# Kernel optimization log

Hardware: AMD Instinct MI355X
Metric: run time of the kernel (lower is better)

## Reference

```python
import jax, jax.numpy as jnp
import numpy as np

B = 524288
HID = 128
EPS = 1e-3

def _linear_params(key, fan_in, fan_out):
    k1, k2 = jax.random.split(key)
    s = 1.0 / np.sqrt(fan_in)
    W = jax.random.uniform(k1, (fan_out, fan_in), jnp.float32, -s, s)
    b = jax.random.uniform(k2, (fan_out,), jnp.float32, -s, s)
    return W, b

def _mlp(x, W1, b1, W2, b2):
    # Linear -> Tanh -> Linear (torch weight layout [out,in])
    h = jnp.tanh(x @ W1.T + b1)
    return h @ W2.T + b2

def setup_inputs() -> dict:
    key = jax.random.key(0)
    ks = jax.random.split(key, 12)
    q = jax.random.normal(ks[0], (B, 2), jnp.float32)
    qd = jax.random.normal(ks[1], (B, 2), jnp.float32)
    u = jax.random.normal(ks[2], (B, 2), jnp.float32)
    Wm1, bm1 = _linear_params(ks[3], 2, HID)
    Wm2, bm2 = _linear_params(ks[4], HID, 4)
    Wc1, bc1 = _linear_params(ks[5], 4, HID)
    Wc2, bc2 = _linear_params(ks[6], HID, 4)
    Wg1, bg1 = _linear_params(ks[7], 2, HID)
    Wg2, bg2 = _linear_params(ks[8], HID, 2)
    Wt1, bt1 = _linear_params(ks[9], 6, HID)
    Wt2, bt2 = _linear_params(ks[10], HID, 2)
    return dict(q=q, qd=qd, u=u,
                Wm1=Wm1, bm1=bm1, Wm2=Wm2, bm2=bm2,
                Wc1=Wc1, bc1=bc1, Wc2=Wc2, bc2=bc2,
                Wg1=Wg1, bg1=bg1, Wg2=Wg2, bg2=bg2,
                Wt1=Wt1, bt1=bt1, Wt2=Wt2, bt2=bt2)

def reference(q, qd, u,
              Wm1, bm1, Wm2, bm2,
              Wc1, bc1, Wc2, bc2,
              Wg1, bg1, Wg2, bg2,
              Wt1, bt1, Wt2, bt2):
    b = q.shape[0]
    # SPD mass matrix: M = tril(L) tril(L)^T + eps*I, L from MLP(q)
    L = _mlp(q, Wm1, bm1, Wm2, bm2).reshape(b, 2, 2)
    L = jnp.tril(L)
    I = jnp.eye(2, dtype=q.dtype)
    M = jnp.einsum('bik,bjk->bij', L, L) + EPS * I
    # Coriolis matrix from [q, qd]
    C = _mlp(jnp.concatenate([q, qd], axis=-1), Wc1, bc1, Wc2, bc2).reshape(b, 2, 2)
    # Gravity vector from q
    g = _mlp(q, Wg1, bg1, Wg2, bg2)
    # Non-conservative torque from [q, qd, u]
    tau_nc = _mlp(jnp.concatenate([q, qd, u], axis=-1), Wt1, bt1, Wt2, bt2)
    rhs = u - jnp.einsum('bij,bj->bi', C, qd) - g - tau_nc
    qdd = jnp.linalg.solve(M, rhs[..., None])[..., 0]
    return (qdd, M, C, g, tau_nc)
```

## Files before the change

### kernel.cpp

```cpp
#include <hip/hip_runtime.h>

#define HID 128
#define EPSM 1e-3f
#define KLOG2E 2.8853900817779268f

typedef __fp16 h2 __attribute__((ext_vector_type(2)));
typedef __attribute__((address_space(4))) const float cfloat;

__device__ __forceinline__ h2 as_h2(float f){ union U{float f; h2 h;} u; u.f = f; return u.h; }
__device__ __forceinline__ float h2_bits(h2 h){ union U{h2 h; float f;} u; u.h = h; return u.f; }

__device__ __forceinline__ float fdot2f(h2 a, h2 b, float c){
#if __has_builtin(__builtin_amdgcn_fdot2)
    return __builtin_amdgcn_fdot2(a, b, c, false);
#else
    return fmaf((float)a.x, (float)b.x, fmaf((float)a.y, (float)b.y, c));
#endif
}
__device__ __forceinline__ h2 pkrtz(float a, float b){
#if __has_builtin(__builtin_amdgcn_cvt_pkrtz)
    return __builtin_amdgcn_cvt_pkrtz(a, b);
#else
    h2 r; r.x = (__fp16)a; r.y = (__fp16)b; return r;
#endif
}
__device__ __forceinline__ float aexp2(float x){
#if __has_builtin(__builtin_amdgcn_exp2f)
    return __builtin_amdgcn_exp2f(x);
#else
    return __expf(0.6931471805599453f * x);
#endif
}
__device__ __forceinline__ float arcp(float x){
#if __has_builtin(__builtin_amdgcn_rcpf)
    return __builtin_amdgcn_rcpf(x);
#else
    return 1.0f / x;
#endif
}
__device__ __forceinline__ float tanh_s(float a){
    float t = aexp2(a);
    float r = arcp(t + 1.0f);
    return fmaf(-2.0f, r, 1.0f);
}

__device__ __forceinline__ float h2f(float a, float b){
    h2 h; h.x = (__fp16)a; h.y = (__fp16)b; return h2_bits(h);
}

__global__ void phynn_pack(const float* __restrict__ Wm1, const float* __restrict__ bm1,
                           const float* __restrict__ Wm2, const float* __restrict__ bm2,
                           const float* __restrict__ Wc1, const float* __restrict__ bc1,
                           const float* __restrict__ Wc2, const float* __restrict__ bc2,
                           const float* __restrict__ Wg1, const float* __restrict__ bg1,
                           const float* __restrict__ Wg2, const float* __restrict__ bg2,
                           const float* __restrict__ Wt1, const float* __restrict__ bt1,
                           const float* __restrict__ Wt2, const float* __restrict__ bt2,
                           float* __restrict__ P)
{
    const float k = KLOG2E;
    int p = threadIdx.x;
    if (p < 64) {
        int n0 = 2*p, n1 = 2*p + 1;
        float* o = P + p * 40;
        o[0]  = k*Wm1[2*n0];   o[1]  = k*Wm1[2*n0+1]; o[2]  = k*bm1[n0];     o[3]  = Wm2[n0];
        o[4]  = Wm2[256+n0];   o[5]  = Wm2[384+n0];   o[6]  = k*Wm1[2*n1];   o[7]  = k*Wm1[2*n1+1];
        o[8]  = k*bm1[n1];     o[9]  = Wm2[n1];       o[10] = Wm2[256+n1];   o[11] = Wm2[384+n1];
        o[12] = h2f(k*Wg1[2*n0], k*Wg1[2*n0+1]);
        o[13] = h2f(k*Wg1[2*n1], k*Wg1[2*n1+1]);
        o[14] = k*bg1[n0];     o[15] = k*bg1[n1];
        o[16] = h2f(Wg2[n0],      Wg2[n1]);
        o[17] = h2f(Wg2[128+n0],  Wg2[128+n1]);
        o[18] = h2f(k*Wc1[4*n0],   k*Wc1[4*n0+1]);
        o[19] = h2f(k*Wc1[4*n0+2], k*Wc1[4*n0+3]);
        o[20] = h2f(k*Wc1[4*n1],   k*Wc1[4*n1+1]);
        o[21] = h2f(k*Wc1[4*n1+2], k*Wc1[4*n1+3]);
        o[22] = k*bc1[n0];     o[23] = k*bc1[n1];
        o[24] = h2f(Wc2[n0],      Wc2[n1]);
        o[25] = h2f(Wc2[128+n0],  Wc2[128+n1]);
        o[26] = h2f(Wc2[256+n0],  Wc2[256+n1]);
        o[27] = h2f(Wc2[384+n0],  Wc2[384+n1]);
        o[28] = h2f(k*Wt1[6*n0],   k*Wt1[6*n0+1]);
        o[29] = h2f(k*Wt1[6*n0+2], k*Wt1[6*n0+3]);
        o[30] = h2f(k*Wt1[6*n0+4], k*Wt1[6*n0+5]);
        o[31] = k*bt1[n0];
        o[32] = h2f(k*Wt1[6*n1],   k*Wt1[6*n1+1]);
        o[33] = h2f(k*Wt1[6*n1+2], k*Wt1[6*n1+3]);
        o[34] = h2f(k*Wt1[6*n1+4], k*Wt1[6*n1+5]);
        o[35] = k*bt1[n1];
        o[36] = h2f(Wt2[n0],     Wt2[n1]);
        o[37] = h2f(Wt2[128+n0], Wt2[128+n1]);
        o[38] = 0.f; o[39] = 0.f;
    }
    if (p == 64) {
        float* t = P + 2560;
        t[0] = bm2[0]; t[1] = bm2[1]; t[2]  = bm2[2]; t[3]  = bm2[3];
        t[4] = bc2[0]; t[5] = bc2[1]; t[6]  = bc2[2]; t[7]  = bc2[3];
        t[8] = bg2[0]; t[9] = bg2[1]; t[10] = bt2[0]; t[11] = bt2[1];
    }
}

#define NPE 2

__global__ __launch_bounds__(256, 4) void phynn_main(
    const float2* __restrict__ q, const float2* __restrict__ qd, const float2* __restrict__ u,
    const float* __restrict__ P, float* __restrict__ out, int B)
{
    cfloat* W = (cfloat*)(unsigned long long)P;

    const int half = B >> 1;
    const int tid  = blockIdx.x * 256 + threadIdx.x;
    if (tid >= half) return;

    int e[NPE];
    e[0] = tid;
    e[1] = tid + half;

    float q0[NPE], q1[NPE], d0[NPE], d1[NPE], u0[NPE], u1[NPE];
    h2 qh[NPE], dh[NPE], uh[NPE];
    #pragma unroll
    for (int s = 0; s < NPE; ++s) {
        float2 vq = q[e[s]];  q0[s] = vq.x; q1[s] = vq.y;
        float2 vd = qd[e[s]]; d0[s] = vd.x; d1[s] = vd.y;
        float2 vu = u[e[s]];  u0[s] = vu.x; u1[s] = vu.y;
        qh[s] = pkrtz(q0[s], q1[s]);
        dh[s] = pkrtz(d0[s], d1[s]);
        uh[s] = pkrtz(u0[s], u1[s]);
    }

    float aL0[NPE] = {}, aL2[NPE] = {}, aL3[NPE] = {};
    float aC0[NPE] = {}, aC1[NPE] = {}, aC2[NPE] = {}, aC3[NPE] = {};
    float aG0[NPE] = {}, aG1[NPE] = {};
    float aT0[NPE] = {}, aT1[NPE] = {};

    #pragma unroll 2
    for (int p = 0; p < 64; ++p) {
        cfloat* w = W + p * 40;
        const float w0  = w[0],  w1  = w[1],  w2  = w[2],  w3  = w[3];
        const float w4  = w[4],  w5  = w[5],  w6  = w[6],  w7  = w[7];
        const float w8  = w[8],  w9  = w[9],  w10 = w[10], w11 = w[11];
        const float w12 = w[12], w13 = w[13], w14 = w[14], w15 = w[15];
        const float w16 = w[16], w17 = w[17], w18 = w[18], w19 = w[19];
        const float w20 = w[20], w21 = w[21], w22 = w[22], w23 = w[23];
        const float w24 = w[24], w25 = w[25], w26 = w[26], w27 = w[27];
        const float w28 = w[28], w29 = w[29], w30 = w[30], w31 = w[31];
        const float w32 = w[32], w33 = w[33], w34 = w[34], w35 = w[35];
        const float w36 = w[36], w37 = w[37];

        const h2 gw0 = as_h2(w12), gw1 = as_h2(w13);
        const h2 gl0 = as_h2(w16), gl1 = as_h2(w17);
        const h2 c0a = as_h2(w18), c0b = as_h2(w19);
        const h2 c1a = as_h2(w20), c1b = as_h2(w21);
        const h2 cl0 = as_h2(w24), cl1 = as_h2(w25), cl2 = as_h2(w26), cl3 = as_h2(w27);
        const h2 t0a = as_h2(w28), t0b = as_h2(w29), t0c = as_h2(w30);
        const h2 t1a = as_h2(w32), t1b = as_h2(w33), t1c = as_h2(w34);
        const h2 tl0 = as_h2(w36), tl1 = as_h2(w37);

        #pragma unroll
        for (int s = 0; s < NPE; ++s) {
            float am0 = fmaf(w0, q0[s], fmaf(w1, q1[s], w2));
            float am1 = fmaf(w6, q0[s], fmaf(w7, q1[s], w8));
            float hm0 = tanh_s(am0);
            float hm1 = tanh_s(am1);
            aL0[s] = fmaf(w3,  hm0, fmaf(w9,  hm1, aL0[s]));
            aL2[s] = fmaf(w4,  hm0, fmaf(w10, hm1, aL2[s]));
            aL3[s] = fmaf(w5,  hm0, fmaf(w11, hm1, aL3[s]));
            float ag0 = fdot2f(gw0, qh[s], w14);
            float ag1 = fdot2f(gw1, qh[s], w15);
            h2 hg = pkrtz(tanh_s(ag0), tanh_s(ag1));
            aG0[s] = fdot2f(gl0, hg, aG0[s]);
            aG1[s] = fdot2f(gl1, hg, aG1[s]);
            float ac0 = fdot2f(c0a, qh[s], fdot2f(c0b, dh[s], w22));
            float ac1 = fdot2f(c1a, qh[s], fdot2f(c1b, dh[s], w23));
            h2 hc = pkrtz(tanh_s(ac0), tanh_s(ac1));
            aC0[s] = fdot2f(cl0, hc, aC0[s]);
            aC1[s] = fdot2f(cl1, hc, aC1[s]);
            aC2[s] = fdot2f(cl2, hc, aC2[s]);
            aC3[s] = fdot2f(cl3, hc, aC3[s]);
            float at0 = fdot2f(t0a, qh[s], fdot2f(t0b, dh[s], fdot2f(t0c, uh[s], w31)));
            float at1 = fdot2f(t1a, qh[s], fdot2f(t1b, dh[s], fdot2f(t1c, uh[s], w35)));
            h2 ht = pkrtz(tanh_s(at0), tanh_s(at1));
            aT0[s] = fdot2f(tl0, ht, aT0[s]);
            aT1[s] = fdot2f(tl1, ht, aT1[s]);
        }
    }

    cfloat* bt_ = W + 2560;
    const float bm2x = bt_[0], bm2z = bt_[2], bm2w = bt_[3];
    const float bc2x = bt_[4], bc2y = bt_[5], bc2z = bt_[6], bc2w = bt_[7];
    const float bg2x = bt_[8], bg2y = bt_[9], bt2x = bt_[10], bt2y = bt_[11];

    float*  outf  = out;
    float2* o_qdd = (float2*)outf;
    float4* o_M   = (float4*)(outf + (size_t)2 * B);
    float4* o_C   = (float4*)(outf + (size_t)6 * B);
    float2* o_g   = (float2*)(outf + (size_t)10 * B);
    float2* o_t   = (float2*)(outf + (size_t)12 * B);

    #pragma unroll
    for (int s = 0; s < NPE; ++s) {
        float l00 = aL0[s] + bm2x;
        float l10 = aL2[s] + bm2z;
        float l11 = aL3[s] + bm2w;
        float M00 = fmaf(l00, l00, EPSM);
        float M01 = l00 * l10;
        float M11 = fmaf(l10, l10, fmaf(l11, l11, EPSM));

        float C00 = aC0[s] + bc2x;
        float C01 = aC1[s] + bc2y;
        float C10 = aC2[s] + bc2z;
        float C11 = aC3[s] + bc2w;

        float g0 = aG0[s] + bg2x;
        float g1 = aG1[s] + bg2y;
        float t0 = aT0[s] + bt2x;
        float t1 = aT1[s] + bt2y;

        float rhs0 = u0[s] - fmaf(C00, d0[s], C01 * d1[s]) - g0 - t0;
        float rhs1 = u1[s] - fmaf(C10, d0[s], C11 * d1[s]) - g1 - t1;

        float det = fmaf(M00, M11, -(M01 * M01));
        float r0  = arcp(det);
        float rdet = r0 * fmaf(-det, r0, 2.0f);
        float qdd0 = fmaf(M11, rhs0, -(M01 * rhs1)) * rdet;
        float qdd1 = fmaf(M00, rhs1, -(M01 * rhs0)) * rdet;

        o_qdd[e[s]] = make_float2(qdd0, qdd1);
        o_M[e[s]]   = make_float4(M00, M01, M01, M11);
        o_C[e[s]]   = make_float4(C00, C01, C10, C11);
        o_g[e[s]]   = make_float2(g0, g1);
        o_t[e[s]]   = make_float2(t0, t1);
    }
}

extern "C" void kernel_launch(void* const* d_in, const int* in_sizes, int n_in,
                              void* d_out, int out_size, void* d_ws, size_t ws_size,
                              hipStream_t stream)
{
    const float* q   = (const float*)d_in[0];
    const float* qd  = (const float*)d_in[1];
    const float* u   = (const float*)d_in[2];
    const float* Wm1 = (const float*)d_in[3];
    const float* bm1 = (const float*)d_in[4];
    const float* Wm2 = (const float*)d_in[5];
    const float* bm2 = (const float*)d_in[6];
    const float* Wc1 = (const float*)d_in[7];
    const float* bc1 = (const float*)d_in[8];
    const float* Wc2 = (const float*)d_in[9];
    const float* bc2 = (const float*)d_in[10];
    const float* Wg1 = (const float*)d_in[11];
    const float* bg1 = (const float*)d_in[12];
    const float* Wg2 = (const float*)d_in[13];
    const float* bg2 = (const float*)d_in[14];
    const float* Wt1 = (const float*)d_in[15];
    const float* bt1 = (const float*)d_in[16];
    const float* Wt2 = (const float*)d_in[17];
    const float* bt2 = (const float*)d_in[18];

    const int B = in_sizes[0] / 2;
    float* P = (float*)d_ws;

    hipLaunchKernelGGL(phynn_pack, dim3(1), dim3(128), 0, stream,
                       Wm1, bm1, Wm2, bm2, Wc1, bc1, Wc2, bc2,
                       Wg1, bg1, Wg2, bg2, Wt1, bt1, Wt2, bt2, P);

    const int half   = B / 2;
    const int blocks = (half + 255) / 256;
    hipLaunchKernelGGL(phynn_main, dim3(blocks), dim3(256), 0, stream,
                       (const float2*)q, (const float2*)qd, (const float2*)u,
                       P, (float*)d_out, B);
}
```

Baseline: 90.78 us.

## Batch four tanh reciprocals into one and process one element per thread

```diff
diff --git a/kernel.cpp b/kernel.cpp
--- a/kernel.cpp
+++ b/kernel.cpp
@@ -1,6 +1,5 @@
 #include <hip/hip_runtime.h>
 
-#define HID 128
 #define EPSM 1e-3f
 #define KLOG2E 2.8853900817779268f
 
@@ -38,10 +37,33 @@
     return 1.0f / x;
 #endif
 }
-__device__ __forceinline__ float tanh_s(float a){
-    float t = aexp2(a);
-    float r = arcp(t + 1.0f);
-    return fmaf(-2.0f, r, 1.0f);
+__device__ __forceinline__ float fmed3(float a, float lo, float hi){
+#if __has_builtin(__builtin_amdgcn_fmed3f)
+    return __builtin_amdgcn_fmed3f(a, lo, hi);
+#else
+    return fminf(fmaxf(a, lo), hi);
+#endif
+}
+
+__device__ __forceinline__ void tanh4(float a0, float a1, float a2, float a3,
+                                      float& h0, float& h1, float& h2o, float& h3o){
+    const float C = 28.85f;
+    float t0 = aexp2(fmed3(a0, -C, C));
+    float t1 = aexp2(fmed3(a1, -C, C));
+    float t2 = aexp2(fmed3(a2, -C, C));
+    float t3 = aexp2(fmed3(a3, -C, C));
+    float p0 = t0 + 1.0f, p1 = t1 + 1.0f, p2 = t2 + 1.0f, p3 = t3 + 1.0f;
+    float m01 = p0 * p1, m23 = p2 * p3;
+    float m = m01 * m23;
+    union { float f; unsigned u; } s; s.f = m; s.u = 0x7EF311C3u - s.u;
+    float r = s.f;
+    r = r * fmaf(-m, r, 2.0f);
+    r = r * fmaf(-m, r, 2.0f);
+    float I01 = r * m23, I23 = r * m01;
+    h0  = fmaf(-2.0f, I01 * p1, 1.0f);
+    h1  = fmaf(-2.0f, I01 * p0, 1.0f);
+    h2o = fmaf(-2.0f, I23 * p3, 1.0f);
+    h3o = fmaf(-2.0f, I23 * p2, 1.0f);
 }
 
 __device__ __forceinline__ float h2f(float a, float b){
@@ -100,38 +122,26 @@
     }
 }
 
-#define NPE 2
-
-__global__ __launch_bounds__(256, 4) void phynn_main(
+__global__ __launch_bounds__(256, 8) void phynn_main(
     const float2* __restrict__ q, const float2* __restrict__ qd, const float2* __restrict__ u,
     const float* __restrict__ P, float* __restrict__ out, int B)
 {
     cfloat* W = (cfloat*)(unsigned long long)P;
 
-    const int half = B >> 1;
-    const int tid  = blockIdx.x * 256 + threadIdx.x;
-    if (tid >= half) return;
-
-    int e[NPE];
-    e[0] = tid;
-    e[1] = tid + half;
-
-    float q0[NPE], q1[NPE], d0[NPE], d1[NPE], u0[NPE], u1[NPE];
-    h2 qh[NPE], dh[NPE], uh[NPE];
-    #pragma unroll
-    for (int s = 0; s < NPE; ++s) {
-        float2 vq = q[e[s]];  q0[s] = vq.x; q1[s] = vq.y;
-        float2 vd = qd[e[s]]; d0[s] = vd.x; d1[s] = vd.y;
-        float2 vu = u[e[s]];  u0[s] = vu.x; u1[s] = vu.y;
-        qh[s] = pkrtz(q0[s], q1[s]);
-        dh[s] = pkrtz(d0[s], d1[s]);
-        uh[s] = pkrtz(u0[s], u1[s]);
-    }
-
-    float aL0[NPE] = {}, aL2[NPE] = {}, aL3[NPE] = {};
-    float aC0[NPE] = {}, aC1[NPE] = {}, aC2[NPE] = {}, aC3[NPE] = {};
-    float aG0[NPE] = {}, aG1[NPE] = {};
-    float aT0[NPE] = {}, aT1[NPE] = {};
+    const int tid = blockIdx.x * 256 + threadIdx.x;
+    if (tid >= B) return;
+
+    float2 vq = q[tid];  const float q0 = vq.x, q1 = vq.y;
+    float2 vd = qd[tid]; const float d0 = vd.x, d1 = vd.y;
+    float2 vu = u[tid];  const float u0 = vu.x, u1 = vu.y;
+    const h2 qh = pkrtz(q0, q1);
+    const h2 dh = pkrtz(d0, d1);
+    const h2 uh = pkrtz(u0, u1);
+
+    float aL0 = 0.f, aL2 = 0.f, aL3 = 0.f;
+    float aC0 = 0.f, aC1 = 0.f, aC2 = 0.f, aC3 = 0.f;
+    float aG0 = 0.f, aG1 = 0.f;
+    float aT0 = 0.f, aT1 = 0.f;
 
     #pragma unroll 2
     for (int p = 0; p < 64; ++p) {
@@ -156,39 +166,65 @@
         const h2 t1a = as_h2(w32), t1b = as_h2(w33), t1c = as_h2(w34);
         const h2 tl0 = as_h2(w36), tl1 = as_h2(w37);
 
-        #pragma unroll
-        for (int s = 0; s < NPE; ++s) {
-            float am0 = fmaf(w0, q0[s], fmaf(w1, q1[s], w2));
-            float am1 = fmaf(w6, q0[s], fmaf(w7, q1[s], w8));
-            float hm0 = tanh_s(am0);
-            float hm1 = tanh_s(am1);
-            aL0[s] = fmaf(w3,  hm0, fmaf(w9,  hm1, aL0[s]));
-            aL2[s] = fmaf(w4,  hm0, fmaf(w10, hm1, aL2[s]));
-            aL3[s] = fmaf(w5,  hm0, fmaf(w11, hm1, aL3[s]));
-            float ag0 = fdot2f(gw0, qh[s], w14);
-            float ag1 = fdot2f(gw1, qh[s], w15);
-            h2 hg = pkrtz(tanh_s(ag0), tanh_s(ag1));
-            aG0[s] = fdot2f(gl0, hg, aG0[s]);
-            aG1[s] = fdot2f(gl1, hg, aG1[s]);
-            float ac0 = fdot2f(c0a, qh[s], fdot2f(c0b, dh[s], w22));
-            float ac1 = fdot2f(c1a, qh[s], fdot2f(c1b, dh[s], w23));
-            h2 hc = pkrtz(tanh_s(ac0), tanh_s(ac1));
-            aC0[s] = fdot2f(cl0, hc, aC0[s]);
-            aC1[s] = fdot2f(cl1, hc, aC1[s]);
-            aC2[s] = fdot2f(cl2, hc, aC2[s]);
-            aC3[s] = fdot2f(cl3, hc, aC3[s]);
-            float at0 = fdot2f(t0a, qh[s], fdot2f(t0b, dh[s], fdot2f(t0c, uh[s], w31)));
-            float at1 = fdot2f(t1a, qh[s], fdot2f(t1b, dh[s], fdot2f(t1c, uh[s], w35)));
-            h2 ht = pkrtz(tanh_s(at0), tanh_s(at1));
-            aT0[s] = fdot2f(tl0, ht, aT0[s]);
-            aT1[s] = fdot2f(tl1, ht, aT1[s]);
-        }
+        float am0 = fmaf(w0, q0, fmaf(w1, q1, w2));
+        float am1 = fmaf(w6, q0, fmaf(w7, q1, w8));
+        float ag0 = fdot2f(gw0, qh, w14);
+        float ag1 = fdot2f(gw1, qh, w15);
+        float ac0 = fdot2f(c0a, qh, fdot2f(c0b, dh, w22));
+        float ac1 = fdot2f(c1a, qh, fdot2f(c1b, dh, w23));
+        float at0 = fdot2f(t0a, qh, fdot2f(t0b, dh, fdot2f(t0c, uh, w31)));
+        float at1 = fdot2f(t1a, qh, fdot2f(t1b, dh, fdot2f(t1c, uh, w35)));
+
+        float hm0, hm1, hg0, hg1, hc0, hc1, ht0, ht1;
+        tanh4(am0, am1, ag0, ag1, hm0, hm1, hg0, hg1);
+        tanh4(ac0, ac1, at0, at1, hc0, hc1, ht0, ht1);
+
+        aL0 = fmaf(w3,  hm0, fmaf(w9,  hm1, aL0));
+        aL2 = fmaf(w4,  hm0, fmaf(w10, hm1, aL2));
+        aL3 = fmaf(w5,  hm0, fmaf(w11, hm1, aL3));
+        h2 hg = pkrtz(hg0, hg1);
+        h2 hc = pkrtz(hc0, hc1);
+        h2 ht = pkrtz(ht0, ht1);
+        aG0 = fdot2f(gl0, hg, aG0);
+        aG1 = fdot2f(gl1, hg, aG1);
+        aC0 = fdot2f(cl0, hc, aC0);
+        aC1 = fdot2f(cl1, hc, aC1);
+        aC2 = fdot2f(cl2, hc, aC2);
+        aC3 = fdot2f(cl3, hc, aC3);
+        aT0 = fdot2f(tl0, ht, aT0);
+        aT1 = fdot2f(tl1, ht, aT1);
     }
 
     cfloat* bt_ = W + 2560;
     const float bm2x = bt_[0], bm2z = bt_[2], bm2w = bt_[3];
     const float bc2x = bt_[4], bc2y = bt_[5], bc2z = bt_[6], bc2w = bt_[7];
     const float bg2x = bt_[8], bg2y = bt_[9], bt2x = bt_[10], bt2y = bt_[11];
+
+    float l00 = aL0 + bm2x;
+    float l10 = aL2 + bm2z;
+    float l11 = aL3 + bm2w;
+    float M00 = fmaf(l00, l00, EPSM);
+    float M01 = l00 * l10;
+    float M11 = fmaf(l10, l10, fmaf(l11, l11, EPSM));
+
+    float C00 = aC0 + bc2x;
+    float C01 = aC1 + bc2y;
+    float C10 = aC2 + bc2z;
+    float C11 = aC3 + bc2w;
+
+    float g0 = aG0 + bg2x;
+    float g1 = aG1 + bg2y;
+    float t0 = aT0 + bt2x;
+    float t1 = aT1 + bt2y;
+
+    float rhs0 = u0 - fmaf(C00, d0, C01 * d1) - g0 - t0;
+    float rhs1 = u1 - fmaf(C10, d0, C11 * d1) - g1 - t1;
+
+    float det = fmaf(M00, M11, -(M01 * M01));
+    float r0  = arcp(det);
+    float rdet = r0 * fmaf(-det, r0, 2.0f);
+    float qdd0 = fmaf(M11, rhs0, -(M01 * rhs1)) * rdet;
+    float qdd1 = fmaf(M00, rhs1, -(M01 * rhs0)) * rdet;
 
     float*  outf  = out;
     float2* o_qdd = (float2*)outf;
@@ -197,40 +233,11 @@
     float2* o_g   = (float2*)(outf + (size_t)10 * B);
     float2* o_t   = (float2*)(outf + (size_t)12 * B);
 
-    #pragma unroll
-    for (int s = 0; s < NPE; ++s) {
-        float l00 = aL0[s] + bm2x;
-        float l10 = aL2[s] + bm2z;
-        float l11 = aL3[s] + bm2w;
-        float M00 = fmaf(l00, l00, EPSM);
-        float M01 = l00 * l10;
-        float M11 = fmaf(l10, l10, fmaf(l11, l11, EPSM));
-
-        float C00 = aC0[s] + bc2x;
-        float C01 = aC1[s] + bc2y;
-        float C10 = aC2[s] + bc2z;
-        float C11 = aC3[s] + bc2w;
-
-        float g0 = aG0[s] + bg2x;
-        float g1 = aG1[s] + bg2y;
-        float t0 = aT0[s] + bt2x;
-        float t1 = aT1[s] + bt2y;
-
-        float rhs0 = u0[s] - fmaf(C00, d0[s], C01 * d1[s]) - g0 - t0;
-        float rhs1 = u1[s] - fmaf(C10, d0[s], C11 * d1[s]) - g1 - t1;
-
-        float det = fmaf(M00, M11, -(M01 * M01));
-        float r0  = arcp(det);
-        float rdet = r0 * fmaf(-det, r0, 2.0f);
-        float qdd0 = fmaf(M11, rhs0, -(M01 * rhs1)) * rdet;
-        float qdd1 = fmaf(M00, rhs1, -(M01 * rhs0)) * rdet;
-
-        o_qdd[e[s]] = make_float2(qdd0, qdd1);
-        o_M[e[s]]   = make_float4(M00, M01, M01, M11);
-        o_C[e[s]]   = make_float4(C00, C01, C10, C11);
-        o_g[e[s]]   = make_float2(g0, g1);
-        o_t[e[s]]   = make_float2(t0, t1);
-    }
+    o_qdd[tid] = make_float2(qdd0, qdd1);
+    o_M[tid]   = make_float4(M00, M01, M01, M11);
+    o_C[tid]   = make_float4(C00, C01, C10, C11);
+    o_g[tid]   = make_float2(g0, g1);
+    o_t[tid]   = make_float2(t0, t1);
 }
 
 extern "C" void kernel_launch(void* const* d_in, const int* in_sizes, int n_in,
@@ -264,8 +271,7 @@
                        Wm1, bm1, Wm2, bm2, Wc1, bc1, Wc2, bc2,
                        Wg1, bg1, Wg2, bg2, Wt1, bt1, Wt2, bt2, P);
 
-    const int half   = B / 2;
-    const int blocks = (half + 255) / 256;
+    const int blocks = (B + 255) / 256;
     hipLaunchKernelGGL(phynn_main, dim3(blocks), dim3(256), 0, stream,
                        (const float2*)q, (const float2*)qd, (const float2*)u,
                        P, (float*)d_out, B);
```

After: 105.8 us. 16.5% more time.

## Split hidden dimension across two thread halves with shared-memory reduction

Applied to the files above, without the earlier changes.

```diff
diff --git a/kernel.cpp b/kernel.cpp
--- a/kernel.cpp
+++ b/kernel.cpp
@@ -1,6 +1,5 @@
 #include <hip/hip_runtime.h>
 
-#define HID 128
 #define EPSM 1e-3f
 #define KLOG2E 2.8853900817779268f
 
@@ -101,16 +100,20 @@
 }
 
 #define NPE 2
-
-__global__ __launch_bounds__(256, 4) void phynn_main(
+#define NACC 11
+
+__global__ __launch_bounds__(256, 8) void phynn_main(
     const float2* __restrict__ q, const float2* __restrict__ qd, const float2* __restrict__ u,
     const float* __restrict__ P, float* __restrict__ out, int B)
 {
+    __shared__ float red[128][2*NACC + 1];
+
     cfloat* W = (cfloat*)(unsigned long long)P;
 
     const int half = B >> 1;
-    const int tid  = blockIdx.x * 256 + threadIdx.x;
-    if (tid >= half) return;
+    const int idx  = threadIdx.x & 127;
+    const int kh   = threadIdx.x >> 7;
+    const int tid  = blockIdx.x * 128 + idx;
 
     int e[NPE];
     e[0] = tid;
@@ -133,8 +136,9 @@
     float aG0[NPE] = {}, aG1[NPE] = {};
     float aT0[NPE] = {}, aT1[NPE] = {};
 
+    const int p0 = kh << 5;
     #pragma unroll 2
-    for (int p = 0; p < 64; ++p) {
+    for (int p = p0; p < p0 + 32; ++p) {
         cfloat* w = W + p * 40;
         const float w0  = w[0],  w1  = w[1],  w2  = w[2],  w3  = w[3];
         const float w4  = w[4],  w5  = w[5],  w6  = w[6],  w7  = w[7];
@@ -185,6 +189,32 @@
         }
     }
 
+    if (kh) {
+        float* r = red[idx];
+        r[0]  = aL0[0]; r[1]  = aL2[0]; r[2]  = aL3[0];
+        r[3]  = aG0[0]; r[4]  = aG1[0];
+        r[5]  = aC0[0]; r[6]  = aC1[0]; r[7]  = aC2[0]; r[8]  = aC3[0];
+        r[9]  = aT0[0]; r[10] = aT1[0];
+        r[11] = aL0[1]; r[12] = aL2[1]; r[13] = aL3[1];
+        r[14] = aG0[1]; r[15] = aG1[1];
+        r[16] = aC0[1]; r[17] = aC1[1]; r[18] = aC2[1]; r[19] = aC3[1];
+        r[20] = aT0[1]; r[21] = aT1[1];
+    }
+    __syncthreads();
+    if (kh) return;
+
+    {
+        const float* r = red[idx];
+        aL0[0] += r[0];  aL2[0] += r[1];  aL3[0] += r[2];
+        aG0[0] += r[3];  aG1[0] += r[4];
+        aC0[0] += r[5];  aC1[0] += r[6];  aC2[0] += r[7];  aC3[0] += r[8];
+        aT0[0] += r[9];  aT1[0] += r[10];
+        aL0[1] += r[11]; aL2[1] += r[12]; aL3[1] += r[13];
+        aG0[1] += r[14]; aG1[1] += r[15];
+        aC0[1] += r[16]; aC1[1] += r[17]; aC2[1] += r[18]; aC3[1] += r[19];
+        aT0[1] += r[20]; aT1[1] += r[21];
+    }
+
     cfloat* bt_ = W + 2560;
     const float bm2x = bt_[0], bm2z = bt_[2], bm2w = bt_[3];
     const float bc2x = bt_[4], bc2y = bt_[5], bc2z = bt_[6], bc2w = bt_[7];
@@ -264,8 +294,7 @@
                        Wm1, bm1, Wm2, bm2, Wc1, bc1, Wc2, bc2,
                        Wg1, bg1, Wg2, bg2, Wt1, bt1, Wt2, bt2, P);
 
-    const int half   = B / 2;
-    const int blocks = (half + 255) / 256;
+    const int blocks = (B / 2 + 127) / 128;
     hipLaunchKernelGGL(phynn_main, dim3(blocks), dim3(256), 0, stream,
                        (const float2*)q, (const float2*)qd, (const float2*)u,
                        P, (float*)d_out, B);
```

New measurement: 102.6 us. 13.0% more time.
